# Optimization experiments

Measured on AMD Instinct MI355X. Metric: run time of the kernel, lower is better.

## Reference

```python
import jax, jax.numpy as jnp
import numpy as np

N, E, D_IN, HID, HEADS, D_OUT = 50000, 500000, 128, 64, 8, 8
NEG_SLOPE = 0.2


def gat_conv(x, src, dst, W, a_src, a_dst, bias, concat):
    """PyG GATConv forward (with self-loops already appended to src/dst).
    x: [N, Fin], W: [Fin, H*C], a_src/a_dst: [H, C], bias: [H*C] or [C].
    """
    n = x.shape[0]
    H, C = a_src.shape
    h = (x @ W).reshape(n, H, C)                      # [N, H, C]
    alpha_src = jnp.sum(h * a_src, axis=-1)           # [N, H]
    alpha_dst = jnp.sum(h * a_dst, axis=-1)           # [N, H]
    e = alpha_src[src] + alpha_dst[dst]               # [E, H]
    e = jax.nn.leaky_relu(e, NEG_SLOPE)
    # segment softmax over destination node (every node has a self-loop)
    m = jax.ops.segment_max(e, dst, num_segments=n)   # [N, H]
    w = jnp.exp(e - m[dst])                           # [E, H]
    denom = jax.ops.segment_sum(w, dst, num_segments=n)
    alpha = w / (denom[dst] + 1e-16)                  # [E, H]
    msg = h[src] * alpha[..., None]                   # [E, H, C]
    out = jax.ops.segment_sum(msg, dst, num_segments=n)  # [N, H, C]
    out = out.reshape(n, H * C) if concat else out.mean(axis=1)
    return out + bias


def setup_inputs() -> dict:
    key = jax.random.key(0)
    ks = jax.random.split(key, 10)
    x = jax.random.normal(ks[0], (N, D_IN), dtype=jnp.float32)
    edge_index = jax.random.randint(ks[1], (2, E), 0, N, dtype=jnp.int32)
    s1 = 1.0 / np.sqrt(D_IN)
    s2 = 1.0 / np.sqrt(HID * HEADS)
    W1 = jax.random.normal(ks[2], (D_IN, HEADS * HID), dtype=jnp.float32) * s1
    a_src1 = jax.random.normal(ks[3], (HEADS, HID), dtype=jnp.float32) * 0.1
    a_dst1 = jax.random.normal(ks[4], (HEADS, HID), dtype=jnp.float32) * 0.1
    b1 = jnp.zeros((HEADS * HID,), dtype=jnp.float32)
    W2 = jax.random.normal(ks[5], (HEADS * HID, D_OUT), dtype=jnp.float32) * s2
    a_src2 = jax.random.normal(ks[6], (1, D_OUT), dtype=jnp.float32) * 0.1
    a_dst2 = jax.random.normal(ks[7], (1, D_OUT), dtype=jnp.float32) * 0.1
    b2 = jnp.zeros((D_OUT,), dtype=jnp.float32)
    return {"x": x, "edge_index": edge_index, "W1": W1, "a_src1": a_src1,
            "a_dst1": a_dst1, "b1": b1, "W2": W2, "a_src2": a_src2,
            "a_dst2": a_dst2, "b2": b2}


def reference(x, edge_index, W1, a_src1, a_dst1, b1, W2, a_src2, a_dst2, b2):
    n = x.shape[0]
    loops = jnp.arange(n, dtype=edge_index.dtype)
    src = jnp.concatenate([edge_index[0], loops])  # PyG adds self-loops
    dst = jnp.concatenate([edge_index[1], loops])
    h = jax.nn.relu(gat_conv(x, src, dst, W1, a_src1, a_dst1, b1, concat=True))
    out = gat_conv(h, src, dst, W2, a_src2, a_dst2, b2, concat=False)
    return out
```

## Files before the change

kernel.cpp:

```cpp
#include <hip/hip_runtime.h>
#include <stdint.h>

#define LEAKY(x) ((x) > 0.f ? (x) : 0.2f * (x))

typedef short bf16x8 __attribute__((ext_vector_type(8)));
typedef float f32x4 __attribute__((ext_vector_type(4)));

__device__ inline float2 bf2_to_f2(uint32_t p) {
    return make_float2(__uint_as_float(p << 16), __uint_as_float(p & 0xffff0000u));
}
__device__ inline uint32_t pack_bf2(float x, float y) {
    uint32_t xb = __float_as_uint(x), yb = __float_as_uint(y);
    xb += 0x7fff + ((xb >> 16) & 1);
    yb += 0x7fff + ((yb >> 16) & 1);
    return (xb >> 16) | (yb & 0xffff0000u);
}
__device__ inline ushort to_bf16(float v) {
    uint32_t b = __float_as_uint(v);
    b += 0x7fff + ((b >> 16) & 1);
    return (ushort)(b >> 16);
}


__global__ __launch_bounds__(256) void degree_w1t_kernel(const int* __restrict__ dst,
                                                         int* __restrict__ deg, int E,
                                                         int nEb,
                                                         const float* __restrict__ W,
                                                         ushort* __restrict__ WT) {
    if ((int)blockIdx.x < nEb) {
        int e = blockIdx.x * 256 + threadIdx.x;
        if (e < E) atomicAdd(&deg[dst[e]], 1);
    } else {
        int bb = blockIdx.x - nEb;
        int c = bb * 64 + (threadIdx.x & 63);
        int k0 = (threadIdx.x >> 6) * 32;
        #pragma unroll
        for (int j = 0; j < 32; ++j)
            WT[(size_t)c * 128 + k0 + j] = to_bf16(W[(size_t)(k0 + j) * 512 + c]);
    }
}


__global__ __launch_bounds__(1024) void scan1_kernel(const int* __restrict__ deg,
                                                     int* __restrict__ off,
                                                     int* __restrict__ bsum, int n) {
    __shared__ int wsum[16];
    int b = blockIdx.x, tid = threadIdx.x;
    int lane = tid & 63, wid = tid >> 6;
    int i0 = b * 4096 + tid * 4;
    int v0 = 0, v1 = 0, v2 = 0, v3 = 0;
    if (i0 + 3 < n) {
        int4 q = *(const int4*)(deg + i0);
        v0 = q.x; v1 = q.y; v2 = q.z; v3 = q.w;
    } else {
        if (i0 + 0 < n) v0 = deg[i0];
        if (i0 + 1 < n) v1 = deg[i0 + 1];
        if (i0 + 2 < n) v2 = deg[i0 + 2];
        if (i0 + 3 < n) v3 = deg[i0 + 3];
    }
    int s = v0 + v1 + v2 + v3;
    int x = s;
    #pragma unroll
    for (int d2 = 1; d2 < 64; d2 <<= 1) {
        int y = __shfl_up(x, d2);
        if (lane >= d2) x += y;
    }
    if (lane == 63) wsum[wid] = x;
    __syncthreads();
    if (tid < 16) {
        int t = wsum[tid];
        #pragma unroll
        for (int d2 = 1; d2 < 16; d2 <<= 1) {
            int y = __shfl_up(t, d2, 16);
            if (tid >= d2) t += y;
        }
        wsum[tid] = t;
    }
    __syncthreads();
    int wbase = wid ? wsum[wid - 1] : 0;
    int pre = wbase + (x - s);
    if (i0 < n)     off[i0]     = pre;
    if (i0 + 1 < n) off[i0 + 1] = pre + v0;
    if (i0 + 2 < n) off[i0 + 2] = pre + v0 + v1;
    if (i0 + 3 < n) off[i0 + 3] = pre + v0 + v1 + v2;
    if (tid == 0) bsum[b] = wsum[15];
}

__global__ void scan2_kernel(int* __restrict__ bsum, int* __restrict__ off, int nb, int n) {
    int tid = threadIdx.x;
    int v = (tid < nb) ? bsum[tid] : 0;
    int x = v;
    #pragma unroll
    for (int d2 = 1; d2 < 64; d2 <<= 1) {
        int y = __shfl_up(x, d2);
        if (tid >= d2) x += y;
    }
    if (tid < nb) bsum[tid] = x - v;
    if (tid == 63) off[n] = x;
}

__global__ __launch_bounds__(1024) void scan3_kernel(int* __restrict__ off,
                                                     const int* __restrict__ bsum, int n) {
    int b = blockIdx.x;
    int base = bsum[b];
    if (base == 0) return;
    int i = b * 4096 + threadIdx.x * 4;
    if (i + 3 < n) {
        int4 q = *(int4*)(off + i);
        q.x += base; q.y += base; q.z += base; q.w += base;
        *(int4*)(off + i) = q;
    } else {
        #pragma unroll
        for (int k = 0; k < 4; ++k)
            if (i + k < n) off[i + k] += base;
    }
}

__global__ void scatter_kernel(const int* __restrict__ src, const int* __restrict__ dst,
                               const int* __restrict__ off, int* __restrict__ cursor,
                               int* __restrict__ csr_src, int E) {
    int e = blockIdx.x * blockDim.x + threadIdx.x;
    if (e < E) {
        int d = dst[e];
        int p = atomicAdd(&cursor[d], 1);
        csr_src[off[d] + p] = src[e];
    }
}


__global__ __launch_bounds__(256) void gemm1_kernel(const float* __restrict__ x,
                                                    const ushort* __restrict__ W1T,
                                                    const float* __restrict__ a_src,
                                                    const float* __restrict__ a_dst,
                                                    uint32_t* __restrict__ h1,
                                                    float* __restrict__ asrc1,
                                                    float* __restrict__ adst1, int N) {
    __shared__ __align__(16) ushort As[128][128];
    __shared__ __align__(16) ushort Bs[128][128];
    int tid = threadIdx.x;
    int row0 = blockIdx.x * 128;

    {
        int g = tid & 15;
        int r4 = tid >> 4;
        #pragma unroll
        for (int pass = 0; pass < 8; ++pass) {
            int r = r4 + pass * 16;
            int gr = row0 + r;
            float4 v0 = make_float4(0.f, 0.f, 0.f, 0.f), v1 = v0;
            if (gr < N) {
                v0 = *(const float4*)(x + (size_t)gr * 128 + g * 8);
                v1 = *(const float4*)(x + (size_t)gr * 128 + g * 8 + 4);
            }
            uint4 pk = make_uint4(pack_bf2(v0.x, v0.y), pack_bf2(v0.z, v0.w),
                                  pack_bf2(v1.x, v1.y), pack_bf2(v1.z, v1.w));
            *(uint4*)&As[r][(g ^ (r & 7)) * 8] = pk;
        }
    }
    __syncthreads();

    int wave = tid >> 6, lane = tid & 63;
    int wr = wave >> 1, wc = wave & 1;
    int lg = lane >> 4, lr = lane & 15;

    for (int cb = 0; cb < 4; ++cb) {
        int c0 = cb * 128;
        {
            int g = tid & 15;
            int r4 = tid >> 4;
            #pragma unroll
            for (int pass = 0; pass < 8; ++pass) {
                int r = r4 + pass * 16;
                uint4 q = *(const uint4*)(W1T + (size_t)(c0 + r) * 128 + g * 8);
                *(uint4*)&Bs[r][(g ^ (r & 7)) * 8] = q;
            }
        }
        __syncthreads();

        f32x4 acc[4][4] = {};
        #pragma unroll
        for (int kk = 0; kk < 4; ++kk) {
            bf16x8 a[4], b[4];
            int gk = kk * 4 + lg;
            #pragma unroll
            for (int mi = 0; mi < 4; ++mi) {
                int r = wr * 64 + mi * 16 + lr;
                a[mi] = *(const bf16x8*)&As[r][(gk ^ (r & 7)) * 8];
            }
            #pragma unroll
            for (int nj = 0; nj < 4; ++nj) {
                int r = wc * 64 + nj * 16 + lr;
                b[nj] = *(const bf16x8*)&Bs[r][(gk ^ (r & 7)) * 8];
            }
            #pragma unroll
            for (int mi = 0; mi < 4; ++mi)
                #pragma unroll
                for (int nj = 0; nj < 4; ++nj)
                    acc[mi][nj] = __builtin_amdgcn_mfma_f32_16x16x32_bf16(
                        a[mi], b[nj], acc[mi][nj], 0, 0, 0);
        }

        int hh = cb * 2 + wc;
        float as4[4], ad4[4];
        #pragma unroll
        for (int nj = 0; nj < 4; ++nj) {
            as4[nj] = a_src[hh * 64 + nj * 16 + lr];
            ad4[nj] = a_dst[hh * 64 + nj * 16 + lr];
        }
        #pragma unroll
        for (int mi = 0; mi < 4; ++mi) {
            #pragma unroll
            for (int reg = 0; reg < 4; ++reg) {
                int row = row0 + wr * 64 + mi * 16 + lg * 4 + reg;
                float v0 = acc[mi][0][reg], v1 = acc[mi][1][reg];
                float v2 = acc[mi][2][reg], v3 = acc[mi][3][reg];
                float ps = v0 * as4[0] + v1 * as4[1] + v2 * as4[2] + v3 * as4[3];
                float pd = v0 * ad4[0] + v1 * ad4[1] + v2 * ad4[2] + v3 * ad4[3];
                #pragma unroll
                for (int m = 1; m < 16; m <<= 1) {
                    ps += __shfl_xor(ps, m);
                    pd += __shfl_xor(pd, m);
                }
                bool store_row = (row < N);
                if (store_row && lr == 0) {
                    asrc1[(size_t)row * 8 + hh] = ps;
                    adst1[(size_t)row * 8 + hh] = pd;
                }
                float p0 = __shfl_xor(v0, 1), p1 = __shfl_xor(v1, 1);
                float p2 = __shfl_xor(v2, 1), p3 = __shfl_xor(v3, 1);
                if (store_row && (lr & 1) == 0) {
                    size_t base = (size_t)row * 256 + ((c0 + wc * 64 + lr) >> 1);
                    h1[base + 0]  = pack_bf2(v0, p0);
                    h1[base + 8]  = pack_bf2(v1, p1);
                    h1[base + 16] = pack_bf2(v2, p2);
                    h1[base + 24] = pack_bf2(v3, p3);
                }
            }
        }
        __syncthreads();
    }
}


__global__ __launch_bounds__(256) void agg1_fused_kernel(
        const uint4* __restrict__ h1, const float* __restrict__ asrc,
        const float* __restrict__ adst, const int* __restrict__ off,
        const int* __restrict__ csr_src, const float* __restrict__ b1,
        const float* __restrict__ W2, const float* __restrict__ a_src2,
        const float* __restrict__ a_dst2, float* __restrict__ h2,
        float* __restrict__ as2, float* __restrict__ ad2, int N) {
    __shared__ __align__(16) float w2s[64 * 68];
    int tid = threadIdx.x;
    #pragma unroll
    for (int q = 0; q < 4; ++q) {
        float4 v = ((const float4*)W2)[tid * 4 + q];
        int g = tid * 16 + q * 4;
        *(float4*)&w2s[(g >> 6) * 68 + (g & 63)] = v;
    }
    __syncthreads();

    int n = (blockIdx.x * blockDim.x + tid) >> 6;
    int lane = tid & 63;
    if (n >= N) return;
    int hd = lane >> 3;
    float ad = adst[(size_t)n * 8 + hd];
    float acc[8];
    float d;
    {
        float w = __expf(LEAKY(asrc[(size_t)n * 8 + hd] + ad));
        d = w;
        uint4 p = h1[(size_t)n * 64 + lane];
        float2 c0 = bf2_to_f2(p.x), c1 = bf2_to_f2(p.y);
        float2 c2 = bf2_to_f2(p.z), c3 = bf2_to_f2(p.w);
        acc[0] = w * c0.x; acc[1] = w * c0.y; acc[2] = w * c1.x; acc[3] = w * c1.y;
        acc[4] = w * c2.x; acc[5] = w * c2.y; acc[6] = w * c3.x; acc[7] = w * c3.y;
    }
    auto addp = [&](uint4 p, float w) {
        float2 c0 = bf2_to_f2(p.x), c1 = bf2_to_f2(p.y);
        float2 c2 = bf2_to_f2(p.z), c3 = bf2_to_f2(p.w);
        d += w;
        acc[0] += w * c0.x; acc[1] += w * c0.y; acc[2] += w * c1.x; acc[3] += w * c1.y;
        acc[4] += w * c2.x; acc[5] += w * c2.y; acc[6] += w * c3.x; acc[7] += w * c3.y;
    };
    int t = off[n], tend = off[n + 1];
    for (; t + 3 < tend; t += 4) {
        int s0 = csr_src[t], s1 = csr_src[t + 1];
        int s2 = csr_src[t + 2], s3 = csr_src[t + 3];
        uint4 p0 = h1[(size_t)s0 * 64 + lane];
        uint4 p1 = h1[(size_t)s1 * 64 + lane];
        uint4 p2 = h1[(size_t)s2 * 64 + lane];
        uint4 p3 = h1[(size_t)s3 * 64 + lane];
        float w0 = __expf(LEAKY(asrc[(size_t)s0 * 8 + hd] + ad));
        float w1 = __expf(LEAKY(asrc[(size_t)s1 * 8 + hd] + ad));
        float w2 = __expf(LEAKY(asrc[(size_t)s2 * 8 + hd] + ad));
        float w3 = __expf(LEAKY(asrc[(size_t)s3 * 8 + hd] + ad));
        addp(p0, w0); addp(p1, w1); addp(p2, w2); addp(p3, w3);
    }
    for (; t < tend; ++t) {
        int s = csr_src[t];
        uint4 p = h1[(size_t)s * 64 + lane];
        float w = __expf(LEAKY(asrc[(size_t)s * 8 + hd] + ad));
        addp(p, w);
    }
    float inv = 1.f / (d + 1e-16f);
    float4 b0 = *(const float4*)(b1 + lane * 8);
    float4 b4 = *(const float4*)(b1 + lane * 8 + 4);
    float o[8];
    o[0] = fmaxf(acc[0] * inv + b0.x, 0.f);
    o[1] = fmaxf(acc[1] * inv + b0.y, 0.f);
    o[2] = fmaxf(acc[2] * inv + b0.z, 0.f);
    o[3] = fmaxf(acc[3] * inv + b0.w, 0.f);
    o[4] = fmaxf(acc[4] * inv + b4.x, 0.f);
    o[5] = fmaxf(acc[5] * inv + b4.y, 0.f);
    o[6] = fmaxf(acc[6] * inv + b4.z, 0.f);
    o[7] = fmaxf(acc[7] * inv + b4.w, 0.f);
    asm volatile("" ::: "memory");
    const float* wrow = &w2s[lane * 68];
    float pc[8] = {};
    #pragma unroll
    for (int j = 0; j < 8; ++j) {
        float4 wa = *(const float4*)(wrow + j * 8);
        float4 wb = *(const float4*)(wrow + j * 8 + 4);
        float ov = o[j];
        pc[0] += ov * wa.x; pc[1] += ov * wa.y;
        pc[2] += ov * wa.z; pc[3] += ov * wa.w;
        pc[4] += ov * wb.x; pc[5] += ov * wb.y;
        pc[6] += ov * wb.z; pc[7] += ov * wb.w;
    }
    #pragma unroll
    for (int m = 1; m < 64; m <<= 1)
        #pragma unroll
        for (int c = 0; c < 8; ++c)
            pc[c] += __shfl_xor(pc[c], m);
    if (lane < 8) {
        float myv = 0.f;
        #pragma unroll
        for (int c = 0; c < 8; ++c) if (lane == c) myv = pc[c];
        h2[(size_t)n * 8 + lane] = myv;
        if (lane == 0) {
            float pa = 0.f, pb = 0.f;
            #pragma unroll
            for (int c = 0; c < 8; ++c) { pa += pc[c] * a_src2[c]; pb += pc[c] * a_dst2[c]; }
            as2[n] = pa;
            ad2[n] = pb;
        }
    }
}


__global__ __launch_bounds__(256) void agg2_kernel(const float* __restrict__ h2,
                                                   const float* __restrict__ as2,
                                                   const float* __restrict__ ad2,
                                                   const int* __restrict__ off,
                                                   const int* __restrict__ csr_src,
                                                   const float* __restrict__ b2,
                                                   float* __restrict__ out, int N) {
    int gid = blockIdx.x * blockDim.x + threadIdx.x;
    int n = gid >> 3, c = gid & 7;
    if (n >= N) return;
    float adn = ad2[n];
    float e = LEAKY(as2[n] + adn);
    float w = __expf(e);
    float d = w;
    float acc = w * h2[(size_t)n * 8 + c];
    int t0e = off[n], t1e = off[n + 1];
    for (int t = t0e; t < t1e; ++t) {
        int s = csr_src[t];
        float ee = LEAKY(as2[s] + adn);
        float ws = __expf(ee);
        d += ws;
        acc += ws * h2[(size_t)s * 8 + c];
    }
    out[(size_t)n * 8 + c] = acc / (d + 1e-16f) + b2[c];
}


extern "C" void kernel_launch(void* const* d_in, const int* in_sizes, int n_in,
                              void* d_out, int out_size, void* d_ws, size_t ws_size,
                              hipStream_t stream) {
    const float* x      = (const float*)d_in[0];
    const int*   ei     = (const int*)d_in[1];
    const float* W1     = (const float*)d_in[2];
    const float* a_src1 = (const float*)d_in[3];
    const float* a_dst1 = (const float*)d_in[4];
    const float* b1     = (const float*)d_in[5];
    const float* W2     = (const float*)d_in[6];
    const float* a_src2 = (const float*)d_in[7];
    const float* a_dst2 = (const float*)d_in[8];
    const float* b2     = (const float*)d_in[9];

    int N = in_sizes[0] / 128;
    int E = in_sizes[1] / 2;
    const int* src = ei;
    const int* dst = ei + E;

    char* w = (char*)d_ws;
    size_t o = 0;
    auto alloc = [&](size_t bytes) {
        void* p = w + o;
        o = (o + bytes + 255) & ~(size_t)255;
        return p;
    };
    uint32_t* h1     = (uint32_t*)alloc((size_t)N * 256 * 4);
    float*    asrc1  = (float*)alloc((size_t)N * 8 * 4);
    float*    adst1  = (float*)alloc((size_t)N * 8 * 4);
    float*    h2     = (float*)alloc((size_t)N * 8 * 4);
    float*    as2    = (float*)alloc((size_t)N * 4);
    float*    ad2    = (float*)alloc((size_t)N * 4);
    int*      deg    = (int*)alloc((size_t)N * 4);
    int*      offb   = (int*)alloc((size_t)(N + 1) * 4);
    int*      cursor = (int*)alloc((size_t)N * 4);
    int*      csrs   = (int*)alloc((size_t)E * 4);
    ushort*   W1T    = (ushort*)alloc((size_t)512 * 128 * 2);
    int*      bsum   = (int*)alloc(64 * 4);

    hipMemsetAsync(deg, 0, (size_t)N * 4, stream);
    hipMemsetAsync(cursor, 0, (size_t)N * 4, stream);

    int nb = (N + 4095) / 4096;
    int nEb = (E + 255) / 256;
    degree_w1t_kernel<<<nEb + 8, 256, 0, stream>>>(dst, deg, E, nEb, W1, W1T);
    scan1_kernel<<<nb, 1024, 0, stream>>>(deg, offb, bsum, N);
    scan2_kernel<<<1, 64, 0, stream>>>(bsum, offb, nb, N);
    scan3_kernel<<<nb, 1024, 0, stream>>>(offb, bsum, N);
    scatter_kernel<<<nEb, 256, 0, stream>>>(src, dst, offb, cursor, csrs, E);

    gemm1_kernel<<<(N + 127) / 128, 256, 0, stream>>>(x, W1T, a_src1, a_dst1,
                                                      h1, asrc1, adst1, N);
    agg1_fused_kernel<<<((size_t)N * 64 + 255) / 256, 256, 0, stream>>>(
        (const uint4*)h1, asrc1, adst1, offb, csrs, b1, W2, a_src2, a_dst2,
        h2, as2, ad2, N);

    agg2_kernel<<<((size_t)N * 8 + 255) / 256, 256, 0, stream>>>(h2, as2, ad2, offb, csrs, b2,
                                                                 (float*)d_out, N);
}
```

Measured before the change: 199.3 us.

## Fuse CSR scatter into GEMM1 launch and seed cursors from scan offsets

The edge scatter is merged into the GEMM1 kernel as extra blocks, so the GEMM and the CSR build run concurrently in a single launch. scan3 now writes absolute offsets into the cursor array, which removes the cursor memset and the offset read in the scatter. LeakyReLU becomes an fmaxf, and the aggregation accumulators are regrouped as float2. The trade-off is that the scatter blocks reserve the GEMM's 64KB of shared memory, which could lower occupancy for those lightweight blocks.

```diff
diff --git a/kernel.cpp b/kernel.cpp
--- a/kernel.cpp
+++ b/kernel.cpp
@@ -1,7 +1,7 @@
 #include <hip/hip_runtime.h>
 #include <stdint.h>
 
-#define LEAKY(x) ((x) > 0.f ? (x) : 0.2f * (x))
+#define LEAKY(x) fmaxf((x), 0.2f * (x))
 
 typedef short bf16x8 __attribute__((ext_vector_type(8)));
 typedef float f32x4 __attribute__((ext_vector_type(4)));
@@ -100,44 +100,47 @@
 }
 
 __global__ __launch_bounds__(1024) void scan3_kernel(int* __restrict__ off,
+                                                     int* __restrict__ cur,
                                                      const int* __restrict__ bsum, int n) {
     int b = blockIdx.x;
     int base = bsum[b];
-    if (base == 0) return;
     int i = b * 4096 + threadIdx.x * 4;
     if (i + 3 < n) {
         int4 q = *(int4*)(off + i);
         q.x += base; q.y += base; q.z += base; q.w += base;
         *(int4*)(off + i) = q;
+        *(int4*)(cur + i) = q;
     } else {
         #pragma unroll
         for (int k = 0; k < 4; ++k)
-            if (i + k < n) off[i + k] += base;
-    }
-}
-
-__global__ void scatter_kernel(const int* __restrict__ src, const int* __restrict__ dst,
-                               const int* __restrict__ off, int* __restrict__ cursor,
-                               int* __restrict__ csr_src, int E) {
-    int e = blockIdx.x * blockDim.x + threadIdx.x;
-    if (e < E) {
-        int d = dst[e];
-        int p = atomicAdd(&cursor[d], 1);
-        csr_src[off[d] + p] = src[e];
-    }
-}
-
-
-__global__ __launch_bounds__(256) void gemm1_kernel(const float* __restrict__ x,
-                                                    const ushort* __restrict__ W1T,
-                                                    const float* __restrict__ a_src,
-                                                    const float* __restrict__ a_dst,
-                                                    uint32_t* __restrict__ h1,
-                                                    float* __restrict__ asrc1,
-                                                    float* __restrict__ adst1, int N) {
+            if (i + k < n) {
+                int v = off[i + k] + base;
+                off[i + k] = v;
+                cur[i + k] = v;
+            }
+    }
+}
+
+
+__global__ __launch_bounds__(256) void gemm1_scatter_kernel(
+        const float* __restrict__ x, const ushort* __restrict__ W1T,
+        const float* __restrict__ a_src, const float* __restrict__ a_dst,
+        uint32_t* __restrict__ h1, float* __restrict__ asrc1,
+        float* __restrict__ adst1, int N, int nGb,
+        const int* __restrict__ esrc, const int* __restrict__ edst,
+        int* __restrict__ cur, int* __restrict__ csr_src, int E) {
     __shared__ __align__(16) ushort As[128][128];
     __shared__ __align__(16) ushort Bs[128][128];
     int tid = threadIdx.x;
+    if ((int)blockIdx.x >= nGb) {
+        int e = (blockIdx.x - nGb) * 256 + tid;
+        if (e < E) {
+            int d = edst[e];
+            int p = atomicAdd(&cur[d], 1);
+            csr_src[p] = esrc[e];
+        }
+        return;
+    }
     int row0 = blockIdx.x * 128;
 
     {
@@ -264,7 +267,7 @@
     if (n >= N) return;
     int hd = lane >> 3;
     float ad = adst[(size_t)n * 8 + hd];
-    float acc[8];
+    float2 acc2[4];
     float d;
     {
         float w = __expf(LEAKY(asrc[(size_t)n * 8 + hd] + ad));
@@ -272,15 +275,19 @@
         uint4 p = h1[(size_t)n * 64 + lane];
         float2 c0 = bf2_to_f2(p.x), c1 = bf2_to_f2(p.y);
         float2 c2 = bf2_to_f2(p.z), c3 = bf2_to_f2(p.w);
-        acc[0] = w * c0.x; acc[1] = w * c0.y; acc[2] = w * c1.x; acc[3] = w * c1.y;
-        acc[4] = w * c2.x; acc[5] = w * c2.y; acc[6] = w * c3.x; acc[7] = w * c3.y;
+        acc2[0] = make_float2(w * c0.x, w * c0.y);
+        acc2[1] = make_float2(w * c1.x, w * c1.y);
+        acc2[2] = make_float2(w * c2.x, w * c2.y);
+        acc2[3] = make_float2(w * c3.x, w * c3.y);
     }
     auto addp = [&](uint4 p, float w) {
         float2 c0 = bf2_to_f2(p.x), c1 = bf2_to_f2(p.y);
         float2 c2 = bf2_to_f2(p.z), c3 = bf2_to_f2(p.w);
         d += w;
-        acc[0] += w * c0.x; acc[1] += w * c0.y; acc[2] += w * c1.x; acc[3] += w * c1.y;
-        acc[4] += w * c2.x; acc[5] += w * c2.y; acc[6] += w * c3.x; acc[7] += w * c3.y;
+        acc2[0].x += w * c0.x; acc2[0].y += w * c0.y;
+        acc2[1].x += w * c1.x; acc2[1].y += w * c1.y;
+        acc2[2].x += w * c2.x; acc2[2].y += w * c2.y;
+        acc2[3].x += w * c3.x; acc2[3].y += w * c3.y;
     };
     int t = off[n], tend = off[n + 1];
     for (; t + 3 < tend; t += 4) {
@@ -306,14 +313,14 @@
     float4 b0 = *(const float4*)(b1 + lane * 8);
     float4 b4 = *(const float4*)(b1 + lane * 8 + 4);
     float o[8];
-    o[0] = fmaxf(acc[0] * inv + b0.x, 0.f);
-    o[1] = fmaxf(acc[1] * inv + b0.y, 0.f);
-    o[2] = fmaxf(acc[2] * inv + b0.z, 0.f);
-    o[3] = fmaxf(acc[3] * inv + b0.w, 0.f);
-    o[4] = fmaxf(acc[4] * inv + b4.x, 0.f);
-    o[5] = fmaxf(acc[5] * inv + b4.y, 0.f);
-    o[6] = fmaxf(acc[6] * inv + b4.z, 0.f);
-    o[7] = fmaxf(acc[7] * inv + b4.w, 0.f);
+    o[0] = fmaxf(acc2[0].x * inv + b0.x, 0.f);
+    o[1] = fmaxf(acc2[0].y * inv + b0.y, 0.f);
+    o[2] = fmaxf(acc2[1].x * inv + b0.z, 0.f);
+    o[3] = fmaxf(acc2[1].y * inv + b0.w, 0.f);
+    o[4] = fmaxf(acc2[2].x * inv + b4.x, 0.f);
+    o[5] = fmaxf(acc2[2].y * inv + b4.y, 0.f);
+    o[6] = fmaxf(acc2[3].x * inv + b4.z, 0.f);
+    o[7] = fmaxf(acc2[3].y * inv + b4.w, 0.f);
     asm volatile("" ::: "memory");
     const float* wrow = &w2s[lane * 68];
     float pc[8] = {};
@@ -409,24 +416,25 @@
     float*    ad2    = (float*)alloc((size_t)N * 4);
     int*      deg    = (int*)alloc((size_t)N * 4);
     int*      offb   = (int*)alloc((size_t)(N + 1) * 4);
-    int*      cursor = (int*)alloc((size_t)N * 4);
+    int*      cur    = (int*)alloc((size_t)N * 4);
     int*      csrs   = (int*)alloc((size_t)E * 4);
     ushort*   W1T    = (ushort*)alloc((size_t)512 * 128 * 2);
     int*      bsum   = (int*)alloc(64 * 4);
 
     hipMemsetAsync(deg, 0, (size_t)N * 4, stream);
-    hipMemsetAsync(cursor, 0, (size_t)N * 4, stream);
 
     int nb = (N + 4095) / 4096;
     int nEb = (E + 255) / 256;
+    int nGb = (N + 127) / 128;
     degree_w1t_kernel<<<nEb + 8, 256, 0, stream>>>(dst, deg, E, nEb, W1, W1T);
     scan1_kernel<<<nb, 1024, 0, stream>>>(deg, offb, bsum, N);
     scan2_kernel<<<1, 64, 0, stream>>>(bsum, offb, nb, N);
-    scan3_kernel<<<nb, 1024, 0, stream>>>(offb, bsum, N);
-    scatter_kernel<<<nEb, 256, 0, stream>>>(src, dst, offb, cursor, csrs, E);
-
-    gemm1_kernel<<<(N + 127) / 128, 256, 0, stream>>>(x, W1T, a_src1, a_dst1,
-                                                      h1, asrc1, adst1, N);
+    scan3_kernel<<<nb, 1024, 0, stream>>>(offb, cur, bsum, N);
+
+    gemm1_scatter_kernel<<<nGb + nEb, 256, 0, stream>>>(
+        x, W1T, a_src1, a_dst1, h1, asrc1, adst1, N, nGb,
+        src, dst, cur, csrs, E);
+
     agg1_fused_kernel<<<((size_t)N * 64 + 255) / 256, 256, 0, stream>>>(
         (const uint4*)h1, asrc1, adst1, offb, csrs, b1, W2, a_src2, a_dst2,
         h2, as2, ad2, N);
```

New measurement: 173.7 us. -12.9%, faster.
